# Optimization experiments

Measured on AMD Instinct MI355X. Metric: run time of the kernel, lower is better.

The kernel has to match this reference:

```python
import jax, jax.numpy as jnp
import numpy as np

B, W, D = 8, 1024, 1024
HEADS, KDIM, VDIM = 16, 64, 64


def setup_inputs() -> dict:
    key = jax.random.key(0)
    k1, k2, k3, k4 = jax.random.split(key, 4)
    # he_normal-ish scaling for weights
    s = (2.0 / D) ** 0.5
    return {
        "inputs": jax.random.normal(k1, (B, W, D), dtype=jnp.float32),
        "Wq": jax.random.normal(k2, (D, HEADS * KDIM), dtype=jnp.float32) * s,
        "Wk": jax.random.normal(k3, (D, HEADS * KDIM), dtype=jnp.float32) * s,
        "Wv": jax.random.normal(k4, (D, HEADS * VDIM), dtype=jnp.float32) * s,
    }


def reference(inputs, Wq, Wk, Wv):
    # Self-attention: memory = inputs
    bsz, win, _ = inputs.shape
    # DenseHeads: linear projection, reshaped to (B, W, heads, head_units)
    q = (inputs @ Wq).reshape(bsz, win, HEADS, KDIM)
    k = (inputs @ Wk).reshape(bsz, win, HEADS, KDIM)
    v = (inputs @ Wv).reshape(bsz, win, HEADS, VDIM)
    scale = KDIM ** (-0.5)
    # scores[b,q,h,m] = sum_k Q[b,q,h,k] * K[b,m,h,k]
    scores = jnp.einsum("bqhk,bmhk->bqhm", q, k) * scale
    attn = jax.nn.softmax(scores, axis=-1)
    # out[b,q,h,v] = sum_m attn[b,q,h,m] * V[b,m,h,v]
    out = jnp.einsum("bqhm,bmhv->bqhv", attn, v)
    return out
```

## Files before the change

### kernel.cpp

```cpp
#include <hip/hip_runtime.h>
#include <stdint.h>


using bf16x8 = __attribute__((ext_vector_type(8))) __bf16;
using f32x4  = __attribute__((ext_vector_type(4))) float;
using f16x4  = __attribute__((ext_vector_type(4))) _Float16;

union frag_u  { uint4 u4; bf16x8 f; };
union vfrag_u { uint2 u2; f16x4 f; };
union pfrag_u { unsigned int u[2]; f16x4 f; };

__device__ inline unsigned short f2bf(float x){
  unsigned int u = __float_as_uint(x);
  u += 0x7fffu + ((u >> 16) & 1u);
  return (unsigned short)(u >> 16);
}

__device__ inline unsigned int pkrtz_u32(float a, float b){
  auto r = __builtin_amdgcn_cvt_pkrtz(a, b);
  unsigned int u; __builtin_memcpy(&u, &r, 4); return u;
}

__device__ inline float fexp2(float x){
#if __has_builtin(__builtin_amdgcn_exp2f)
  return __builtin_amdgcn_exp2f(x);
#else
  float r; asm("v_exp_f32 %0, %1\n\ts_nop 0" : "=v"(r) : "v"(x)); return r;
#endif
}

__device__ inline void gl_lds16(const void* g, void* l){
  __builtin_amdgcn_global_load_lds(
      (const __attribute__((address_space(1))) void*)g,
      (__attribute__((address_space(3))) void*)l, 16, 0, 0);
}

#define SBAR() do{ asm volatile("" ::: "memory"); __builtin_amdgcn_s_barrier(); asm volatile("" ::: "memory"); }while(0)
#define VMC(n)  asm volatile("s_waitcnt vmcnt(" #n ")" ::: "memory")

__global__ void cast_all(const float* __restrict__ X,
                         const float* __restrict__ Wq, const float* __restrict__ Wk,
                         const float* __restrict__ Wv,
                         unsigned short* __restrict__ Xb,
                         unsigned short* __restrict__ Wt){
  __shared__ float tile[64][65];
  int bid = blockIdx.x;
  if (bid < 8192){
    int i = (bid * 256 + threadIdx.x) * 4;
    float4 v = *(const float4*)(X + i);
    ushort4 o;
    o.x = f2bf(v.x); o.y = f2bf(v.y); o.z = f2bf(v.z); o.w = f2bf(v.w);
    *(ushort4*)(Xb + i) = o;
    return;
  }
  int id = bid - 8192;
  int proj = id >> 8;
  int rem  = id & 255;
  int kt = rem & 15, nt = rem >> 4;
  const float* Wsrc = (proj == 0) ? Wq : ((proj == 1) ? Wk : Wv);
  int k0 = kt * 64, n0 = nt * 64;
  int tx = threadIdx.x & 63, ty = threadIdx.x >> 6;
  for (int i = 0; i < 16; i++){
    int k = i * 4 + ty;
    tile[k][tx] = Wsrc[(k0 + k) * 1024 + n0 + tx];
  }
  __syncthreads();
  for (int i = 0; i < 16; i++){
    int n = i * 4 + ty;
    Wt[(proj * 1024 + n0 + n) * 1024 + k0 + tx] = f2bf(tile[tx][n]);
  }
}

__global__ __launch_bounds__(1024, 4) void gemm_qkv(
    const unsigned short* __restrict__ Xb,
    const unsigned short* __restrict__ Wt,
    unsigned short* __restrict__ QK,
    unsigned short* __restrict__ Vt){
  __shared__ __align__(16) char Abuf[2][32768];
  __shared__ __align__(16) char Bbuf[2][24576];

  int bid = blockIdx.x;
  int tau = (bid & 7) * 64 + (bid >> 3);
  int by = tau >> 4, bx = tau & 15;
  int tid = threadIdx.x;
  int w = tid >> 6, lane = tid & 63;
  int li = lane & 15, g = lane >> 4;
  int lrow = lane >> 3;
  int wr = w >> 2, wc = w & 3;
  int wu = __builtin_amdgcn_readfirstlane(w);

  int xcol = ((lane & 7) ^ lrow) << 3;
  int aoff0 = (by * 256 + w * 8 + lrow) * 1024 + xcol;
  int aoff1 = (by * 256 + (16 + w) * 8 + lrow) * 1024 + xcol;
  int bseg0 = (w < 8) ? w : (w + 8);
  int bseg1 = w + 8;
  int boff0 = (bx * 192 + bseg0 * 8 + lrow) * 1024 + xcol;
  int boff1 = (bx * 192 + bseg1 * 8 + lrow) * 1024 + xcol;

  int swz  = (li & 7) << 4;
  int colA0 = (g * 16) ^ swz;
  int colA1 = (64 + g * 16) ^ swz;
  int aBase = (wr * 64 + li) * 128;
  int bBase = (wc * 48 + li) * 128;

  f32x4 acc[4][3] = {};
  frag_u bfr[3][2], af[2][2];

#define LDB(buf) do{ \
  _Pragma("unroll") for (int n = 0; n < 3; n++){ \
    bfr[n][0].u4 = *(const uint4*)&Bbuf[buf][bBase + n * 2048 + colA0]; \
    bfr[n][1].u4 = *(const uint4*)&Bbuf[buf][bBase + n * 2048 + colA1]; } }while(0)
#define LDA2(buf, m0) do{ \
  af[0][0].u4 = *(const uint4*)&Abuf[buf][aBase + (m0)     * 2048 + colA0]; \
  af[0][1].u4 = *(const uint4*)&Abuf[buf][aBase + (m0)     * 2048 + colA1]; \
  af[1][0].u4 = *(const uint4*)&Abuf[buf][aBase + (m0 + 1) * 2048 + colA0]; \
  af[1][1].u4 = *(const uint4*)&Abuf[buf][aBase + (m0 + 1) * 2048 + colA1]; }while(0)
#define MFMA6(P) do{ __builtin_amdgcn_s_setprio(1); \
  _Pragma("unroll") for (int kk = 0; kk < 2; kk++) \
  _Pragma("unroll") for (int i = 0; i < 2; i++) \
  _Pragma("unroll") for (int n = 0; n < 3; n++) \
    acc[(P) + i][n] = __builtin_amdgcn_mfma_f32_16x16x32_bf16( \
        af[i][kk].f, bfr[n][kk].f, acc[(P) + i][n], 0, 0, 0); \
  __builtin_amdgcn_s_setprio(0); }while(0)

  gl_lds16(Wt + boff0, &Bbuf[0][bseg0 * 1024]);
  if (wu < 8) gl_lds16(Wt + boff1, &Bbuf[0][bseg1 * 1024]);
  gl_lds16(Xb + aoff0, &Abuf[0][w * 1024]);
  gl_lds16(Xb + aoff1, &Abuf[0][(16 + w) * 1024]);
  gl_lds16(Wt + boff0 + 64, &Bbuf[1][bseg0 * 1024]);
  if (wu < 8){
    gl_lds16(Wt + boff1 + 64, &Bbuf[1][bseg1 * 1024]);
    VMC(2);
  } else {
    VMC(1);
  }
  SBAR();

  for (int t = 0; t < 16; ++t){
    int cur = t & 1, nxt = cur ^ 1;
    LDB(cur);
    LDA2(cur, 0);
    if (t < 15){
      gl_lds16(Xb + aoff0 + (t + 1) * 64, &Abuf[nxt][w * 1024]);
      gl_lds16(Xb + aoff1 + (t + 1) * 64, &Abuf[nxt][(16 + w) * 1024]);
    }
    MFMA6(0);
    SBAR();
    LDA2(cur, 2);
    if (t < 14){
      gl_lds16(Wt + boff0 + (t + 2) * 64, &Bbuf[cur][bseg0 * 1024]);
      if (wu < 8) gl_lds16(Wt + boff1 + (t + 2) * 64, &Bbuf[cur][bseg1 * 1024]);
    }
    MFMA6(2);
    if (t < 14){
      if (wu < 8) { VMC(2); } else { VMC(1); }
    } else if (t == 14) {
      VMC(0);
    }
    SBAR();
  }
#undef LDB
#undef LDA2
#undef MFMA6

  int row0 = by * 256 + wr * 64 + g * 4;
  int bb16 = (by >> 2) * 16;
#pragma unroll
  for (int n = 0; n < 3; n++){
    int cb = bx * 192 + wc * 48 + n * 16;
    if (cb < 2048){
      float sc = (cb < 1024) ? 0.1803368801111f : 1.0f;
#pragma unroll
      for (int m = 0; m < 4; m++){
        int row = row0 + m * 16;
#pragma unroll
        for (int r = 0; r < 4; r++)
          QK[(size_t)(row + r) * 2048 + cb + li] = f2bf(acc[m][n][r] * sc);
      }
    } else {
      int vc = cb + li - 2048;
      int hh = vc >> 6, dd = vc & 63;
#pragma unroll
      for (int m = 0; m < 4; m++){
        int mtok = (row0 + m * 16) & 1023;
        uint2 cv;
        cv.x = pkrtz_u32(acc[m][n][0], acc[m][n][1]);
        cv.y = pkrtz_u32(acc[m][n][2], acc[m][n][3]);
        *(uint2*)(Vt + ((size_t)(bb16 + hh) * 64 + dd) * 1024 + mtok) = cv;
      }
    }
  }
}

__global__ __launch_bounds__(256, 4) void attn(const unsigned short* __restrict__ QK,
                                               const unsigned short* __restrict__ Vt,
                                               float* __restrict__ Out){
  __shared__ __align__(16) unsigned short Kbuf[64 * 64];
  __shared__ __align__(16) unsigned short Vbuf[64 * 64];
  int id = blockIdx.x;
  int bh = id & 127, qb = id >> 7;
  int b = bh >> 4, h = bh & 15;
  int w = threadIdx.x >> 6, lane = threadIdx.x & 63;
  int g = lane >> 4, li = lane & 15;
  int lrow = lane >> 3, lcol = lane & 7;
  int scol = ((lcol ^ lrow) & 7) * 8;

  frag_u qf[2][2];
#pragma unroll
  for (int u = 0; u < 2; u++){
    int tok = b * 1024 + qb * 128 + w * 32 + u * 16 + li;
    const unsigned short* qp = QK + (size_t)tok * 2048 + h * 64 + g * 8;
    qf[u][0].u4 = *(const uint4*)(qp);
    qf[u][1].u4 = *(const uint4*)(qp + 32);
  }

  f32x4 o[2][4] = {};
  f32x4 osum[2] = {};
  const f32x4 bias = {-10.f, -10.f, -10.f, -10.f};
  pfrag_u ones;
  ones.u[0] = 0x3c003c00u; ones.u[1] = 0x3c003c00u;

  const unsigned short* Kg = QK + (size_t)b * 1024 * 2048 + 1024 + h * 64;
  const unsigned short* Vg = Vt + (size_t)bh * 65536;

  for (int mt = 0; mt < 16; mt++){
    int m0 = mt * 64;
    __syncthreads();
    for (int i = 0; i < 2; i++){
      int idx = w * 2 + i;
      int row = idx * 8 + lrow;
      gl_lds16(Kg + (size_t)(m0 + row) * 2048 + scol, Kbuf + idx * 512);
      gl_lds16(Vg + row * 1024 + m0 + scol,           Vbuf + idx * 512);
    }
    __syncthreads();

    f32x4 s[2][4];
#pragma unroll
    for (int u = 0; u < 2; u++)
#pragma unroll
      for (int t = 0; t < 4; t++) s[u][t] = bias;
#pragma unroll
    for (int t = 0; t < 4; t++){
#pragma unroll
      for (int c = 0; c < 2; c++){
        frag_u kf;
        kf.u4 = *(const uint4*)(Kbuf + (t * 16 + li) * 64 + ((((c << 2) + g) ^ (li & 7)) << 3));
        s[0][t] = __builtin_amdgcn_mfma_f32_16x16x32_bf16(kf.f, qf[0][c].f, s[0][t], 0, 0, 0);
        s[1][t] = __builtin_amdgcn_mfma_f32_16x16x32_bf16(kf.f, qf[1][c].f, s[1][t], 0, 0, 0);
      }
    }

    pfrag_u pf[2][4];
#pragma unroll
    for (int u = 0; u < 2; u++){
#pragma unroll
      for (int t = 0; t < 4; t++){
        float p0 = fexp2(s[u][t][0]);
        float p1 = fexp2(s[u][t][1]);
        float p2 = fexp2(s[u][t][2]);
        float p3 = fexp2(s[u][t][3]);
        pf[u][t].u[0] = pkrtz_u32(p0, p1);
        pf[u][t].u[1] = pkrtz_u32(p2, p3);
      }
    }

#pragma unroll
    for (int t = 0; t < 4; t++){
      osum[0] = __builtin_amdgcn_mfma_f32_16x16x16f16(ones.f, pf[0][t].f, osum[0], 0, 0, 0);
      osum[1] = __builtin_amdgcn_mfma_f32_16x16x16f16(ones.f, pf[1][t].f, osum[1], 0, 0, 0);
    }
#pragma unroll
    for (int tv = 0; tv < 4; tv++){
#pragma unroll
      for (int t = 0; t < 4; t++){
        int gg = ((t * 2 + (g >> 1)) ^ (li & 7));
        vfrag_u vf;
        vf.u2 = *(const uint2*)(Vbuf + (tv * 16 + li) * 64 + gg * 8 + (g & 1) * 4);
        o[0][tv] = __builtin_amdgcn_mfma_f32_16x16x16f16(vf.f, pf[0][t].f, o[0][tv], 0, 0, 0);
        o[1][tv] = __builtin_amdgcn_mfma_f32_16x16x16f16(vf.f, pf[1][t].f, o[1][tv], 0, 0, 0);
      }
    }
  }

#pragma unroll
  for (int u = 0; u < 2; u++){
    float inv = 1.f / osum[u][0];
    int tok = b * 1024 + qb * 128 + w * 32 + u * 16 + li;
    float* op = Out + (size_t)tok * 1024 + h * 64 + g * 4;
#pragma unroll
    for (int tv = 0; tv < 4; tv++){
      float4 v4;
      v4.x = o[u][tv][0] * inv; v4.y = o[u][tv][1] * inv;
      v4.z = o[u][tv][2] * inv; v4.w = o[u][tv][3] * inv;
      *(float4*)(op + tv * 16) = v4;
    }
  }
}

extern "C" void kernel_launch(void* const* d_in, const int* in_sizes, int n_in,
                              void* d_out, int out_size, void* d_ws, size_t ws_size,
                              hipStream_t stream) {
  const float* X  = (const float*)d_in[0];
  const float* Wq = (const float*)d_in[1];
  const float* Wk = (const float*)d_in[2];
  const float* Wv = (const float*)d_in[3];
  float* Out = (float*)d_out;
  char* ws = (char*)d_ws;
  unsigned short* Xb = (unsigned short*)(ws);
  unsigned short* Wt = (unsigned short*)(ws + (size_t)16 * 1024 * 1024);
  unsigned short* QK = (unsigned short*)(ws + (size_t)22 * 1024 * 1024);
  unsigned short* Vt = (unsigned short*)(ws + (size_t)54 * 1024 * 1024);

  cast_all<<<8960, 256, 0, stream>>>(X, Wq, Wk, Wv, Xb, Wt);
  gemm_qkv<<<512, 1024, 0, stream>>>(Xb, Wt, QK, Vt);
  attn    <<<1024, 256, 0, stream>>>(QK, Vt, Out);
}
```

Measured before the change: 191.9 us.

## Halve QKV GEMM block to 8 waves with larger per-wave output tiles

The QKV projection GEMM now runs 512-thread blocks (8 waves arranged 4x2) instead of 1024-thread blocks (16 waves arranged 4x4). Each wave computes a 64x96 output tile with 24 accumulators instead of 64x48, so it reuses each loaded A fragment across twice as many MFMAs. The global-to-LDS loads are redistributed evenly across the 8 waves, which removes the wave-dependent branching. The cost is more registers per wave and fewer resident waves to hide latency.

```diff
diff --git a/kernel.cpp b/kernel.cpp
--- a/kernel.cpp
+++ b/kernel.cpp
@@ -71,7 +71,7 @@
   }
 }
 
-__global__ __launch_bounds__(1024, 4) void gemm_qkv(
+__global__ __launch_bounds__(512, 2) void gemm_qkv(
     const unsigned short* __restrict__ Xb,
     const unsigned short* __restrict__ Wt,
     unsigned short* __restrict__ QK,
@@ -86,28 +86,28 @@
   int w = tid >> 6, lane = tid & 63;
   int li = lane & 15, g = lane >> 4;
   int lrow = lane >> 3;
-  int wr = w >> 2, wc = w & 3;
-  int wu = __builtin_amdgcn_readfirstlane(w);
+  int wr = w >> 1, wc = w & 1;
 
   int xcol = ((lane & 7) ^ lrow) << 3;
-  int aoff0 = (by * 256 + w * 8 + lrow) * 1024 + xcol;
-  int aoff1 = (by * 256 + (16 + w) * 8 + lrow) * 1024 + xcol;
-  int bseg0 = (w < 8) ? w : (w + 8);
-  int bseg1 = w + 8;
-  int boff0 = (bx * 192 + bseg0 * 8 + lrow) * 1024 + xcol;
-  int boff1 = (bx * 192 + bseg1 * 8 + lrow) * 1024 + xcol;
+  int aoff[4], boff[3];
+#pragma unroll
+  for (int j = 0; j < 4; j++)
+    aoff[j] = (by * 256 + (j * 8 + w) * 8 + lrow) * 1024 + xcol;
+#pragma unroll
+  for (int j = 0; j < 3; j++)
+    boff[j] = (bx * 192 + (j * 8 + w) * 8 + lrow) * 1024 + xcol;
 
   int swz  = (li & 7) << 4;
   int colA0 = (g * 16) ^ swz;
   int colA1 = (64 + g * 16) ^ swz;
   int aBase = (wr * 64 + li) * 128;
-  int bBase = (wc * 48 + li) * 128;
-
-  f32x4 acc[4][3] = {};
-  frag_u bfr[3][2], af[2][2];
+  int bBase = (wc * 96 + li) * 128;
+
+  f32x4 acc[4][6] = {};
+  frag_u bfr[6][2], af[2][2];
 
 #define LDB(buf) do{ \
-  _Pragma("unroll") for (int n = 0; n < 3; n++){ \
+  _Pragma("unroll") for (int n = 0; n < 6; n++){ \
     bfr[n][0].u4 = *(const uint4*)&Bbuf[buf][bBase + n * 2048 + colA0]; \
     bfr[n][1].u4 = *(const uint4*)&Bbuf[buf][bBase + n * 2048 + colA1]; } }while(0)
 #define LDA2(buf, m0) do{ \
@@ -115,25 +115,21 @@
   af[0][1].u4 = *(const uint4*)&Abuf[buf][aBase + (m0)     * 2048 + colA1]; \
   af[1][0].u4 = *(const uint4*)&Abuf[buf][aBase + (m0 + 1) * 2048 + colA0]; \
   af[1][1].u4 = *(const uint4*)&Abuf[buf][aBase + (m0 + 1) * 2048 + colA1]; }while(0)
-#define MFMA6(P) do{ __builtin_amdgcn_s_setprio(1); \
+#define MFMA12(P) do{ __builtin_amdgcn_s_setprio(1); \
   _Pragma("unroll") for (int kk = 0; kk < 2; kk++) \
   _Pragma("unroll") for (int i = 0; i < 2; i++) \
-  _Pragma("unroll") for (int n = 0; n < 3; n++) \
+  _Pragma("unroll") for (int n = 0; n < 6; n++) \
     acc[(P) + i][n] = __builtin_amdgcn_mfma_f32_16x16x32_bf16( \
         af[i][kk].f, bfr[n][kk].f, acc[(P) + i][n], 0, 0, 0); \
   __builtin_amdgcn_s_setprio(0); }while(0)
 
-  gl_lds16(Wt + boff0, &Bbuf[0][bseg0 * 1024]);
-  if (wu < 8) gl_lds16(Wt + boff1, &Bbuf[0][bseg1 * 1024]);
-  gl_lds16(Xb + aoff0, &Abuf[0][w * 1024]);
-  gl_lds16(Xb + aoff1, &Abuf[0][(16 + w) * 1024]);
-  gl_lds16(Wt + boff0 + 64, &Bbuf[1][bseg0 * 1024]);
-  if (wu < 8){
-    gl_lds16(Wt + boff1 + 64, &Bbuf[1][bseg1 * 1024]);
-    VMC(2);
-  } else {
-    VMC(1);
-  }
+#pragma unroll
+  for (int j = 0; j < 3; j++) gl_lds16(Wt + boff[j], &Bbuf[0][(j * 8 + w) * 1024]);
+#pragma unroll
+  for (int j = 0; j < 4; j++) gl_lds16(Xb + aoff[j], &Abuf[0][(j * 8 + w) * 1024]);
+#pragma unroll
+  for (int j = 0; j < 3; j++) gl_lds16(Wt + boff[j] + 64, &Bbuf[1][(j * 8 + w) * 1024]);
+  VMC(3);
   SBAR();
 
   for (int t = 0; t < 16; ++t){
@@ -141,33 +137,32 @@
     LDB(cur);
     LDA2(cur, 0);
     if (t < 15){
-      gl_lds16(Xb + aoff0 + (t + 1) * 64, &Abuf[nxt][w * 1024]);
-      gl_lds16(Xb + aoff1 + (t + 1) * 64, &Abuf[nxt][(16 + w) * 1024]);
-    }
-    MFMA6(0);
+#pragma unroll
+      for (int j = 0; j < 4; j++)
+        gl_lds16(Xb + aoff[j] + (t + 1) * 64, &Abuf[nxt][(j * 8 + w) * 1024]);
+    }
+    MFMA12(0);
     SBAR();
     LDA2(cur, 2);
     if (t < 14){
-      gl_lds16(Wt + boff0 + (t + 2) * 64, &Bbuf[cur][bseg0 * 1024]);
-      if (wu < 8) gl_lds16(Wt + boff1 + (t + 2) * 64, &Bbuf[cur][bseg1 * 1024]);
-    }
-    MFMA6(2);
-    if (t < 14){
-      if (wu < 8) { VMC(2); } else { VMC(1); }
-    } else if (t == 14) {
-      VMC(0);
-    }
+#pragma unroll
+      for (int j = 0; j < 3; j++)
+        gl_lds16(Wt + boff[j] + (t + 2) * 64, &Bbuf[cur][(j * 8 + w) * 1024]);
+    }
+    MFMA12(2);
+    if (t < 14)      { VMC(3); }
+    else if (t == 14){ VMC(0); }
     SBAR();
   }
 #undef LDB
 #undef LDA2
-#undef MFMA6
+#undef MFMA12
 
   int row0 = by * 256 + wr * 64 + g * 4;
   int bb16 = (by >> 2) * 16;
 #pragma unroll
-  for (int n = 0; n < 3; n++){
-    int cb = bx * 192 + wc * 48 + n * 16;
+  for (int n = 0; n < 6; n++){
+    int cb = bx * 192 + wc * 96 + n * 16;
     if (cb < 2048){
       float sc = (cb < 1024) ? 0.1803368801111f : 1.0f;
 #pragma unroll
@@ -312,6 +307,6 @@
   unsigned short* Vt = (unsigned short*)(ws + (size_t)54 * 1024 * 1024);
 
   cast_all<<<8960, 256, 0, stream>>>(X, Wq, Wk, Wv, Xb, Wt);
-  gemm_qkv<<<512, 1024, 0, stream>>>(Xb, Wt, QK, Vt);
+  gemm_qkv<<<512, 512, 0, stream>>>(Xb, Wt, QK, Vt);
   attn    <<<1024, 256, 0, stream>>>(QK, Vt, Out);
 }
```

Result: slower. 204.6 us (+6.6%).
